# Performance work log

Measured on AMD Instinct MI355X. Metric: run time of the kernel, lower is better.

## Reference

```python
import jax, jax.numpy as jnp
import numpy as np

B, F, G, L, C = 32768, 512, 16, 64, 1000  # batch, feature_dim, n_groups, labels/group, num_classes


def setup_inputs() -> dict:
    key = jax.random.key(0)
    k1, k2, k3, k4, k5 = jax.random.split(key, 5)
    features = jax.random.normal(k1, (B, F), dtype=jnp.float32)
    group_probs = jax.random.uniform(k2, (B, G), dtype=jnp.float32)
    # stacked per-group Linear heads: W[g] is the (L, F) weight of head g, b[g] its bias
    W = jax.random.normal(k3, (G, L, F), dtype=jnp.float32) / np.sqrt(F).astype(np.float32)
    b = jax.random.normal(k4, (G, L), dtype=jnp.float32) * 0.01
    # group_to_labels: label_ids[g, j] = shared class id that head g's j-th output maps to
    label_ids = jax.random.randint(k5, (G, L), 0, C, dtype=jnp.int32)
    return {"features": features, "group_probs": group_probs, "W": W, "b": b,
            "label_ids": label_ids}


def reference(features, group_probs, W, b, label_ids):
    # all per-group linear heads as one batched GEMM: [B,G,L]
    group_logits = jnp.einsum('bf,glf->bgl', features, W) + b
    # weight each group's logits by its group probability
    weighted = group_probs[:, :, None] * group_logits          # [B, G, L]
    # scatter-add into the shared logit tensor (duplicate class ids accumulate)
    flat_idx = label_ids.reshape(-1)                            # [G*L]
    logits = jnp.zeros((features.shape[0], C), dtype=features.dtype)
    logits = logits.at[:, flat_idx].add(weighted.reshape(features.shape[0], -1))
    return logits
```

## Files before the change

### kernel.cpp

```cpp
#include <hip/hip_runtime.h>
#include <stdint.h>

#define B_SZ   32768
#define F_SZ   512
#define G_SZ   16
#define L_SZ   64
#define N_COLS 1024
#define C_SZ   1000
#define M_TILE 64
#define A_STRIDE 520
#define WT_STRIDE 20
#define SMEM_BYTES 81920

typedef __attribute__((ext_vector_type(8))) short short8;
typedef __attribute__((ext_vector_type(4))) float floatx4;

__device__ __forceinline__ unsigned short f2bf(float f) {
    unsigned int x = __float_as_uint(f);
    x += 0x7fffu + ((x >> 16) & 1u);
    return (unsigned short)(x >> 16);
}

__device__ __forceinline__ void barrier_lgkm() {
    __builtin_amdgcn_sched_barrier(0);
    asm volatile("s_waitcnt lgkmcnt(0)" ::: "memory");
    __builtin_amdgcn_s_barrier();
    __builtin_amdgcn_sched_barrier(0);
}

__global__ __launch_bounds__(1024) void build_csr_kernel(const int* __restrict__ label_ids,
                                                         const float* __restrict__ bias,
                                                         int* __restrict__ off,
                                                         int* __restrict__ list,
                                                         float* __restrict__ bias_p,
                                                         unsigned char* __restrict__ g_perm) {
    __shared__ int cnt[1024];
    __shared__ int cur[1024];
    const int t = threadIdx.x;
    cnt[t] = 0;
    __syncthreads();
    const int lbl = label_ids[t];
    atomicAdd(&cnt[lbl], 1);
    __syncthreads();
    int v = cnt[t];
    #pragma unroll
    for (int d = 1; d < 1024; d <<= 1) {
        int u = (t >= d) ? cnt[t - d] : 0;
        __syncthreads();
        v += u;
        cnt[t] = v;
        __syncthreads();
    }
    int ex = (t == 0) ? 0 : cnt[t - 1];
    cur[t] = ex;
    if (t <= C_SZ) off[t] = (t == 0) ? 0 : cnt[t - 1];
    __syncthreads();
    int pos = atomicAdd(&cur[lbl], 1);
    list[pos]   = t;
    bias_p[pos] = bias[t];
    g_perm[pos] = (unsigned char)(t >> 6);
}

__global__ __launch_bounds__(256) void convert_w_kernel(const float* __restrict__ W,
                                                        const int* __restrict__ list,
                                                        unsigned short* __restrict__ Wb) {
    int idx = blockIdx.x * 256 + threadIdx.x;
    int row = idx >> 7;
    int c4  = idx & 127;
    int src = list[row];
    const float4* W4 = (const float4*)W;
    float4 v = W4[src * 128 + c4];
    ushort4 u = make_ushort4(f2bf(v.x), f2bf(v.y), f2bf(v.z), f2bf(v.w));
    ((ushort4*)Wb)[idx] = u;
}

__global__ __launch_bounds__(1024, 4) void mhc_main_kernel(
        const float* __restrict__ feat,
        const float* __restrict__ gp,
        const unsigned short* __restrict__ Wb,
        const float* __restrict__ bias_p,
        const int* __restrict__ off,
        const unsigned char* __restrict__ g_perm,
        float* __restrict__ out)
{
    __shared__ __align__(16) char smem[SMEM_BYTES];
    __shared__ float gp_s[M_TILE * G_SZ];
    __shared__ float bias_s[N_COLS];
    __shared__ unsigned char g_s[N_COLS];

    unsigned short* As = (unsigned short*)smem;
    float* WT = (float*)smem;

    const int t    = threadIdx.x;
    const int wave = t >> 6;
    const int lane = t & 63;
    const int m16  = lane & 15;
    const int quad = lane >> 4;
    const int r0   = blockIdx.x * M_TILE;

    gp_s[t]   = gp[r0 * G_SZ + t];
    bias_s[t] = bias_p[t];
    g_s[t]    = g_perm[t];

    int e0 = 0, e1 = 0;
    if (t < C_SZ) { e0 = off[t]; e1 = off[t + 1]; }

    {
        const float4* f4 = (const float4*)(feat + (size_t)r0 * F_SZ);
        #pragma unroll
        for (int i = 0; i < 8; ++i) {
            int idx = t + i * 1024;
            int row = idx >> 7;
            int c4  = idx & 127;
            float4 v = f4[idx];
            ushort4 u = make_ushort4(f2bf(v.x), f2bf(v.y), f2bf(v.z), f2bf(v.w));
            *(ushort4*)(As + row * A_STRIDE + c4 * 4) = u;
        }
    }
    barrier_lgkm();

    const floatx4 zero = {0.f, 0.f, 0.f, 0.f};
    floatx4 acc[4][4];
    #pragma unroll
    for (int i = 0; i < 4; ++i)
        #pragma unroll
        for (int j = 0; j < 4; ++j) acc[i][j] = zero;

    const unsigned short* aBase = As + m16 * A_STRIDE + quad * 8;
    const unsigned short* bBase = Wb + (size_t)(wave * 64 + m16) * F_SZ + quad * 8;

    #pragma unroll 4
    for (int kt = 0; kt < 16; ++kt) {
        short8 a[4];
        #pragma unroll
        for (int rt = 0; rt < 4; ++rt)
            a[rt] = *(const short8*)(aBase + rt * 16 * A_STRIDE + kt * 32);
        #pragma unroll
        for (int ct = 0; ct < 4; ++ct) {
            short8 b = *(const short8*)(bBase + ct * 16 * F_SZ + kt * 32);
            #pragma unroll
            for (int rt = 0; rt < 4; ++rt)
                acc[rt][ct] = __builtin_amdgcn_mfma_f32_16x16x32_bf16(a[rt], b, acc[rt][ct], 0, 0, 0);
        }
    }

    #pragma unroll
    for (int p = 0; p < 4; ++p) {
        barrier_lgkm();
        #pragma unroll
        for (int ct = 0; ct < 4; ++ct) {
            int col = wave * 64 + ct * 16 + m16;
            int g   = g_s[col];
            float bi = bias_s[col];
            floatx4 w;
            #pragma unroll
            for (int r = 0; r < 4; ++r) {
                int rl = quad * 4 + r;
                w[r] = gp_s[(p * 16 + rl) * G_SZ + g] * (acc[p][ct][r] + bi);
            }
            *(floatx4*)(WT + col * WT_STRIDE + quad * 4) = w;
        }
        barrier_lgkm();
        if (t < C_SZ) {
            floatx4 s0 = zero, s1 = zero, s2 = zero, s3 = zero;
            for (int j = e0; j < e1; ++j) {
                const float* cb = WT + j * WT_STRIDE;
                s0 += *(const floatx4*)(cb + 0);
                s1 += *(const floatx4*)(cb + 4);
                s2 += *(const floatx4*)(cb + 8);
                s3 += *(const floatx4*)(cb + 12);
            }
            size_t rb = (size_t)(r0 + p * 16) * C_SZ + t;
            #pragma unroll
            for (int r = 0; r < 4; ++r) {
                out[rb + (size_t)(r +  0) * C_SZ] = s0[r];
                out[rb + (size_t)(r +  4) * C_SZ] = s1[r];
                out[rb + (size_t)(r +  8) * C_SZ] = s2[r];
                out[rb + (size_t)(r + 12) * C_SZ] = s3[r];
            }
        }
    }
}

extern "C" void kernel_launch(void* const* d_in, const int* in_sizes, int n_in,
                              void* d_out, int out_size, void* d_ws, size_t ws_size,
                              hipStream_t stream) {
    const float* feat  = (const float*)d_in[0];
    const float* gp    = (const float*)d_in[1];
    const float* W     = (const float*)d_in[2];
    const float* bias  = (const float*)d_in[3];
    const int* labels  = (const int*)d_in[4];
    float* out = (float*)d_out;

    unsigned short* Wb = (unsigned short*)d_ws;
    char* base = (char*)d_ws + (1 << 20);
    int* off             = (int*)base;
    int* list            = (int*)(base + 4096);
    float* bias_p        = (float*)(base + 8192);
    unsigned char* g_prm = (unsigned char*)(base + 12288);

    build_csr_kernel<<<1, 1024, 0, stream>>>(labels, bias, off, list, bias_p, g_prm);
    convert_w_kernel<<<(N_COLS * F_SZ / 4) / 256, 256, 0, stream>>>(W, list, Wb);
    mhc_main_kernel<<<B_SZ / M_TILE, 1024, 0, stream>>>(feat, gp, Wb, bias_p, off, g_prm, out);
}
```

Before: 254.5 us.

## Process two row tiles per block and prefetch next tile's features during epilogue

Each block now handles two 64-row tiles. While the first tile's scatter epilogue runs, the next tile's features and group probabilities are prefetched into registers, then converted to bf16 into shared memory. This is meant to hide global load latency and amortize per-block setup. In exchange it adds 32+ prefetch registers under a 1024-thread launch bound and halves the grid to 256 blocks, which may lower occupancy and parallelism.

New measurement: 256.0 us. No clear change (+0.6%).

```diff
diff --git a/kernel.cpp b/kernel.cpp
--- a/kernel.cpp
+++ b/kernel.cpp
@@ -8,6 +8,7 @@
 #define N_COLS 1024
 #define C_SZ   1000
 #define M_TILE 64
+#define TILES_PER_BLK 2
 #define A_STRIDE 520
 #define WT_STRIDE 20
 #define SMEM_BYTES 81920
@@ -96,87 +97,118 @@
     const int lane = t & 63;
     const int m16  = lane & 15;
     const int quad = lane >> 4;
-    const int r0   = blockIdx.x * M_TILE;
-
-    gp_s[t]   = gp[r0 * G_SZ + t];
+
     bias_s[t] = bias_p[t];
     g_s[t]    = g_perm[t];
-
     int e0 = 0, e1 = 0;
     if (t < C_SZ) { e0 = off[t]; e1 = off[t + 1]; }
 
-    {
-        const float4* f4 = (const float4*)(feat + (size_t)r0 * F_SZ);
-        #pragma unroll
-        for (int i = 0; i < 8; ++i) {
-            int idx = t + i * 1024;
-            int row = idx >> 7;
-            int c4  = idx & 127;
-            float4 v = f4[idx];
-            ushort4 u = make_ushort4(f2bf(v.x), f2bf(v.y), f2bf(v.z), f2bf(v.w));
-            *(ushort4*)(As + row * A_STRIDE + c4 * 4) = u;
-        }
-    }
-    barrier_lgkm();
-
-    const floatx4 zero = {0.f, 0.f, 0.f, 0.f};
-    floatx4 acc[4][4];
+    const floatx4* f4g = (const floatx4*)feat;
+    floatx4 pf[8];
+    float pgp = 0.f;
+
     #pragma unroll
-    for (int i = 0; i < 4; ++i)
-        #pragma unroll
-        for (int j = 0; j < 4; ++j) acc[i][j] = zero;
-
-    const unsigned short* aBase = As + m16 * A_STRIDE + quad * 8;
-    const unsigned short* bBase = Wb + (size_t)(wave * 64 + m16) * F_SZ + quad * 8;
-
-    #pragma unroll 4
-    for (int kt = 0; kt < 16; ++kt) {
-        short8 a[4];
-        #pragma unroll
-        for (int rt = 0; rt < 4; ++rt)
-            a[rt] = *(const short8*)(aBase + rt * 16 * A_STRIDE + kt * 32);
-        #pragma unroll
-        for (int ct = 0; ct < 4; ++ct) {
-            short8 b = *(const short8*)(bBase + ct * 16 * F_SZ + kt * 32);
-            #pragma unroll
-            for (int rt = 0; rt < 4; ++rt)
-                acc[rt][ct] = __builtin_amdgcn_mfma_f32_16x16x32_bf16(a[rt], b, acc[rt][ct], 0, 0, 0);
-        }
-    }
-
-    #pragma unroll
-    for (int p = 0; p < 4; ++p) {
-        barrier_lgkm();
-        #pragma unroll
-        for (int ct = 0; ct < 4; ++ct) {
-            int col = wave * 64 + ct * 16 + m16;
-            int g   = g_s[col];
-            float bi = bias_s[col];
-            floatx4 w;
-            #pragma unroll
-            for (int r = 0; r < 4; ++r) {
-                int rl = quad * 4 + r;
-                w[r] = gp_s[(p * 16 + rl) * G_SZ + g] * (acc[p][ct][r] + bi);
-            }
-            *(floatx4*)(WT + col * WT_STRIDE + quad * 4) = w;
+    for (int it = 0; it < TILES_PER_BLK; ++it) {
+        const int tile = blockIdx.x * TILES_PER_BLK + it;
+        const int r0   = tile * M_TILE;
+
+        if (it == 0) {
+            gp_s[t] = gp[(size_t)r0 * G_SZ + t];
+            const floatx4* f4 = f4g + (size_t)r0 * (F_SZ / 4);
+            #pragma unroll
+            for (int i = 0; i < 8; ++i) {
+                int idx = t + i * 1024;
+                int row = idx >> 7;
+                int c4  = idx & 127;
+                floatx4 v = f4[idx];
+                ushort4 u = make_ushort4(f2bf(v[0]), f2bf(v[1]), f2bf(v[2]), f2bf(v[3]));
+                *(ushort4*)(As + row * A_STRIDE + c4 * 4) = u;
+            }
+        } else {
+            barrier_lgkm();
+            gp_s[t] = pgp;
+            #pragma unroll
+            for (int i = 0; i < 8; ++i) {
+                int idx = t + i * 1024;
+                int row = idx >> 7;
+                int c4  = idx & 127;
+                ushort4 u = make_ushort4(f2bf(pf[i][0]), f2bf(pf[i][1]),
+                                         f2bf(pf[i][2]), f2bf(pf[i][3]));
+                *(ushort4*)(As + row * A_STRIDE + c4 * 4) = u;
+            }
         }
         barrier_lgkm();
-        if (t < C_SZ) {
-            floatx4 s0 = zero, s1 = zero, s2 = zero, s3 = zero;
-            for (int j = e0; j < e1; ++j) {
-                const float* cb = WT + j * WT_STRIDE;
-                s0 += *(const floatx4*)(cb + 0);
-                s1 += *(const floatx4*)(cb + 4);
-                s2 += *(const floatx4*)(cb + 8);
-                s3 += *(const floatx4*)(cb + 12);
-            }
-            size_t rb = (size_t)(r0 + p * 16) * C_SZ + t;
-            #pragma unroll
-            for (int r = 0; r < 4; ++r) {
-                out[rb + (size_t)(r +  0) * C_SZ] = s0[r];
-                out[rb + (size_t)(r +  4) * C_SZ] = s1[r];
-                out[rb + (size_t)(r +  8) * C_SZ] = s2[r];
-                out[rb + (size_t)(r + 12) * C_SZ] = s3[r];
+
+        const floatx4 zero = {0.f, 0.f, 0.f, 0.f};
+        floatx4 acc[4][4];
+        #pragma unroll
+        for (int i = 0; i < 4; ++i)
+            #pragma unroll
+            for (int j = 0; j < 4; ++j) acc[i][j] = zero;
+
+        const unsigned short* aBase = As + m16 * A_STRIDE + quad * 8;
+        const unsigned short* bBase = Wb + (size_t)(wave * 64 + m16) * F_SZ + quad * 8;
+
+        #pragma unroll 4
+        for (int kt = 0; kt < 16; ++kt) {
+            short8 a[4];
+            #pragma unroll
+            for (int rt = 0; rt < 4; ++rt)
+                a[rt] = *(const short8*)(aBase + rt * 16 * A_STRIDE + kt * 32);
+            #pragma unroll
+            for (int ct = 0; ct < 4; ++ct) {
+                short8 b = *(const short8*)(bBase + ct * 16 * F_SZ + kt * 32);
+                #pragma unroll
+                for (int rt = 0; rt < 4; ++rt)
+                    acc[rt][ct] = __builtin_amdgcn_mfma_f32_16x16x32_bf16(a[rt], b, acc[rt][ct], 0, 0, 0);
+            }
+        }
+
+        #pragma unroll
+        for (int p = 0; p < 4; ++p) {
+            if (it == 0 && p == 2) {
+                size_t base = (size_t)(tile + 1) * M_TILE * (F_SZ / 4);
+                #pragma unroll
+                for (int i = 0; i < 4; ++i) pf[i] = f4g[base + t + i * 1024];
+                pgp = gp[(size_t)(tile + 1) * M_TILE * G_SZ + t];
+            }
+            if (it == 0 && p == 3) {
+                size_t base = (size_t)(tile + 1) * M_TILE * (F_SZ / 4);
+                #pragma unroll
+                for (int i = 4; i < 8; ++i) pf[i] = f4g[base + t + i * 1024];
+            }
+            barrier_lgkm();
+            #pragma unroll
+            for (int ct = 0; ct < 4; ++ct) {
+                int col = wave * 64 + ct * 16 + m16;
+                int g   = g_s[col];
+                float bi = bias_s[col];
+                floatx4 w;
+                #pragma unroll
+                for (int r = 0; r < 4; ++r) {
+                    int rl = quad * 4 + r;
+                    w[r] = gp_s[(p * 16 + rl) * G_SZ + g] * (acc[p][ct][r] + bi);
+                }
+                *(floatx4*)(WT + col * WT_STRIDE + quad * 4) = w;
+            }
+            barrier_lgkm();
+            if (t < C_SZ) {
+                floatx4 s0 = zero, s1 = zero, s2 = zero, s3 = zero;
+                for (int j = e0; j < e1; ++j) {
+                    const float* cb = WT + j * WT_STRIDE;
+                    s0 += *(const floatx4*)(cb + 0);
+                    s1 += *(const floatx4*)(cb + 4);
+                    s2 += *(const floatx4*)(cb + 8);
+                    s3 += *(const floatx4*)(cb + 12);
+                }
+                size_t rb = (size_t)(r0 + p * 16) * C_SZ + t;
+                #pragma unroll
+                for (int r = 0; r < 4; ++r) {
+                    out[rb + (size_t)(r +  0) * C_SZ] = s0[r];
+                    out[rb + (size_t)(r +  4) * C_SZ] = s1[r];
+                    out[rb + (size_t)(r +  8) * C_SZ] = s2[r];
+                    out[rb + (size_t)(r + 12) * C_SZ] = s3[r];
+                }
             }
         }
     }
@@ -201,5 +233,5 @@
 
     build_csr_kernel<<<1, 1024, 0, stream>>>(labels, bias, off, list, bias_p, g_prm);
     convert_w_kernel<<<(N_COLS * F_SZ / 4) / 256, 256, 0, stream>>>(W, list, Wb);
-    mhc_main_kernel<<<B_SZ / M_TILE, 1024, 0, stream>>>(feat, gp, Wb, bias_p, off, g_prm, out);
-}
+    mhc_main_kernel<<<B_SZ / (M_TILE * TILES_PER_BLK), 1024, 0, stream>>>(feat, gp, Wb, bias_p, off, g_prm, out);
+}
```
